# Optimization experiments

Hardware: AMD Instinct MI355X
Metric: run time of the kernel (lower is better)

## Reference

```python
import jax, jax.numpy as jnp
import numpy as np

D_MODEL = 4096
N_HEADS = 32
N_KV_HEADS = 8
HEAD_DIM = D_MODEL // N_HEADS  # 128
SEQ = 2048
BATCH = 1
ROPE_BASE = 10000.0


def build_rope_cache(max_seq_len, head_dim, base=10000.0):
    half = head_dim // 2
    pos = jnp.arange(max_seq_len, dtype=jnp.float32)
    inv_freqs = 1.0 / (base ** (jnp.arange(half, dtype=jnp.float32) / half))
    angles = pos[:, None] * inv_freqs[None, :]  # (S, half)
    return jnp.cos(angles), jnp.sin(angles)


def apply_rope(t, cos, sin):
    # t: (B, H, S, D); cos/sin: (S, D//2) broadcast over batch & heads.
    t_even = t[..., 0::2]
    t_odd = t[..., 1::2]
    c = cos[None, None, :, :]
    s = sin[None, None, :, :]
    rot_even = t_even * c - t_odd * s
    rot_odd = t_even * s + t_odd * c
    # interleave back into even/odd slots
    return jnp.stack([rot_even, rot_odd], axis=-1).reshape(t.shape)


def setup_inputs() -> dict:
    key = jax.random.key(0)
    kx, kq, kk, kv, ko = jax.random.split(key, 5)
    bound = 1.0 / np.sqrt(D_MODEL)
    x = jax.random.normal(kx, (BATCH, SEQ, D_MODEL), dtype=jnp.float32)
    # torch Linear weights: (out_features, in_features)
    wq = jax.random.uniform(kq, (N_HEADS * HEAD_DIM, D_MODEL), minval=-bound, maxval=bound, dtype=jnp.float32)
    wk = jax.random.uniform(kk, (N_KV_HEADS * HEAD_DIM, D_MODEL), minval=-bound, maxval=bound, dtype=jnp.float32)
    wv = jax.random.uniform(kv, (N_KV_HEADS * HEAD_DIM, D_MODEL), minval=-bound, maxval=bound, dtype=jnp.float32)
    wo = jax.random.uniform(ko, (D_MODEL, D_MODEL), minval=-bound, maxval=bound, dtype=jnp.float32)
    attn_mask = jnp.tril(jnp.ones((SEQ, SEQ), dtype=jnp.int32))[None, None, :, :]
    return {"x": x, "wq": wq, "wk": wk, "wv": wv, "wo": wo, "attn_mask": attn_mask}


def reference(x, wq, wk, wv, wo, attn_mask):
    B, S, _ = x.shape
    cos, sin = build_rope_cache(SEQ, HEAD_DIM, ROPE_BASE)
    cos, sin = cos[:S], sin[:S]
    q = (x @ wq.T).reshape(B, S, N_HEADS, HEAD_DIM).transpose(0, 2, 1, 3)      # (B,H,S,D)
    k = (x @ wk.T).reshape(B, S, N_KV_HEADS, HEAD_DIM).transpose(0, 2, 1, 3)   # (B,Hkv,S,D)
    v = (x @ wv.T).reshape(B, S, N_KV_HEADS, HEAD_DIM).transpose(0, 2, 1, 3)
    q = apply_rope(q, cos, sin)
    k = apply_rope(k, cos, sin)
    n_rep = N_HEADS // N_KV_HEADS
    if n_rep > 1:
        k = jnp.repeat(k, n_rep, axis=1)
        v = jnp.repeat(v, n_rep, axis=1)
    scores = jnp.einsum('bhqd,bhkd->bhqk', q, k) / jnp.sqrt(jnp.float32(HEAD_DIM))
    scores = jnp.where(attn_mask == 0, -jnp.inf, scores)
    attn = jax.nn.softmax(scores, axis=-1)
    out = jnp.einsum('bhqk,bhkd->bhqd', attn, v)
    out = out.transpose(0, 2, 1, 3).reshape(B, S, D_MODEL)
    return out @ wo.T
```

## Files before the change

### kernel.cpp

```cpp
#include <hip/hip_runtime.h>
#include <hip/hip_bf16.h>

typedef float f32x4 __attribute__((ext_vector_type(4)));
typedef __bf16 bf16x4 __attribute__((ext_vector_type(4)));
typedef __bf16 bf16x8 __attribute__((ext_vector_type(8)));

__device__ __forceinline__ void gld_lds16(const void* g, void* l) {
  __builtin_amdgcn_global_load_lds((const __attribute__((address_space(1))) void*)g,
                                   (__attribute__((address_space(3))) void*)l, 16, 0, 0);
}

__global__ void cvt_f32_bf16(const float* __restrict__ in, __bf16* __restrict__ out,
                             int n8) {
  int idx = blockIdx.x * blockDim.x + threadIdx.x;
  if (idx >= n8) return;
  f32x4 a = *(const f32x4*)(in + (size_t)idx * 8);
  f32x4 b = *(const f32x4*)(in + (size_t)idx * 8 + 4);
  bf16x8 o;
#pragma unroll
  for (int j = 0; j < 4; ++j) { o[j] = (__bf16)a[j]; o[4 + j] = (__bf16)b[j]; }
  *(bf16x8*)(out + (size_t)idx * 8) = o;
}

__global__ void build_trig(float* __restrict__ trig) {
  int idx = blockIdx.x * blockDim.x + threadIdx.x;
  if (idx >= 2048 * 64) return;
  int i = idx & 63, s = idx >> 6;
  float ang = (float)s * powf(10000.0f, -(float)i * (1.0f / 64.0f));
  float sn, cs;
  sincosf(ang, &sn, &cs);
  trig[idx * 2] = cs;
  trig[idx * 2 + 1] = sn;
}

__global__ void rope_bf16(__bf16* __restrict__ T, const float* __restrict__ trig,
                          int stride, int nh_mask, int nh_shift, float mul, int total) {
  int idx = blockIdx.x * blockDim.x + threadIdx.x;
  if (idx >= total) return;
  int i = idx & 63;
  int h = (idx >> 6) & nh_mask;
  int s = idx >> (6 + nh_shift);
  float cs = trig[(s * 64 + i) * 2];
  float sn = trig[(s * 64 + i) * 2 + 1];
  __bf16* p = T + (size_t)s * stride + h * 128 + 2 * i;
  float e = (float)p[0], o = (float)p[1];
  p[0] = (__bf16)((e * cs - o * sn) * mul);
  p[1] = (__bf16)((e * sn + o * cs) * mul);
}

__global__ __launch_bounds__(256) void transpose_v(const __bf16* __restrict__ KVb,
                                                   __bf16* __restrict__ Vt) {
  __shared__ __bf16 T[64][72];
  const int tid = threadIdx.x;
  const int s0 = blockIdx.x * 64, d0 = blockIdx.y * 64;
  const int r = tid >> 3, c8 = (tid & 7) * 8;
#pragma unroll
  for (int i = 0; i < 2; ++i) {
    int row = i * 32 + r;
    *(bf16x8*)&T[row][c8] = *(const bf16x8*)&KVb[(size_t)(s0 + row) * 2048 + 1024 + d0 + c8];
  }
  __syncthreads();
#pragma unroll
  for (int i = 0; i < 2; ++i) {
    int drow = i * 32 + r;
    bf16x8 o;
#pragma unroll
    for (int j = 0; j < 8; ++j) o[j] = T[c8 + j][drow];
    *(bf16x8*)&Vt[(size_t)(d0 + drow) * 2048 + s0 + c8] = o;
  }
}

template <int BM, int BN, typename OutT>
__global__ __launch_bounds__(256) void gemm_bf16(const __bf16* __restrict__ A,
                                                 const __bf16* __restrict__ B0,
                                                 const __bf16* __restrict__ B1,
                                                 int Nsplit, OutT* __restrict__ C,
                                                 int M, int N, int K) {
  constexpr int MI = BM / 32, NJ = BN / 32;
  constexpr int RA = BM / 32, RB = BN / 32;
  __shared__ __bf16 As[BM * 64] __attribute__((aligned(16)));
  __shared__ __bf16 Bs[BN * 64] __attribute__((aligned(16)));

  const int tid = threadIdx.x;
  const int lane = tid & 63;
  const int w = tid >> 6;
  const int nwg = gridDim.x * gridDim.y;
  const int orig = blockIdx.y * gridDim.x + blockIdx.x;
  const int wgid = (orig & 7) * (nwg >> 3) + (orig >> 3);
  const int m0 = (wgid % gridDim.x) * BM;
  const int n0 = (wgid / gridDim.x) * BN;
  const int li = lane & 15, lg = lane >> 4;

  const __bf16* bsrc[RB];
#pragma unroll
  for (int i = 0; i < RB; ++i) {
    int slot = i * 256 + w * 64 + lane;
    int row = slot >> 3;
    int sch = (slot & 7) ^ (row & 7);
    int n = n0 + row;
    bsrc[i] = (n < Nsplit ? B0 + (size_t)n * K : B1 + (size_t)(n - Nsplit) * K) +
              sch * 8;
  }
  const __bf16* asrc[RA];
#pragma unroll
  for (int i = 0; i < RA; ++i) {
    int slot = i * 256 + w * 64 + lane;
    int row = slot >> 3;
    int sch = (slot & 7) ^ (row & 7);
    asrc[i] = A + (size_t)(m0 + row) * K + sch * 8;
  }

  const int wr = (w >> 1) * (BM / 2);
  const int wc = (w & 1) * (BN / 2);

  f32x4 acc[MI][NJ] = {};

  for (int k0 = 0; k0 < K; k0 += 64) {
    __syncthreads();
#pragma unroll
    for (int i = 0; i < RA; ++i)
      gld_lds16(asrc[i] + k0, &As[(i * 256 + w * 64) * 8]);
#pragma unroll
    for (int i = 0; i < RB; ++i)
      gld_lds16(bsrc[i] + k0, &Bs[(i * 256 + w * 64) * 8]);
    __syncthreads();

#pragma unroll
    for (int u = 0; u < 2; ++u) {
      bf16x8 af[MI], bfr[NJ];
#pragma unroll
      for (int mi = 0; mi < MI; ++mi)
        af[mi] = *(const bf16x8*)&As[(wr + mi * 16 + li) * 64 +
                                     (((u * 4 + lg) ^ (li & 7)) * 8)];
#pragma unroll
      for (int nj = 0; nj < NJ; ++nj)
        bfr[nj] = *(const bf16x8*)&Bs[(wc + nj * 16 + li) * 64 +
                                      (((u * 4 + lg) ^ (li & 7)) * 8)];
#pragma unroll
      for (int mi = 0; mi < MI; ++mi)
#pragma unroll
        for (int nj = 0; nj < NJ; ++nj)
          acc[mi][nj] = __builtin_amdgcn_mfma_f32_16x16x32_bf16(af[mi], bfr[nj],
                                                                acc[mi][nj], 0, 0, 0);
    }
  }

  const int crow = lg * 4;
#pragma unroll
  for (int mi = 0; mi < MI; ++mi)
#pragma unroll
    for (int nj = 0; nj < NJ; ++nj)
#pragma unroll
      for (int r = 0; r < 4; ++r)
        C[(size_t)(m0 + wr + mi * 16 + crow + r) * N + (n0 + wc + nj * 16 + li)] =
            (OutT)acc[mi][nj][r];
}

__global__ __launch_bounds__(512) void attn_fwd_v6(const __bf16* __restrict__ Q,
                                                   const __bf16* __restrict__ KVb,
                                                   const __bf16* __restrict__ Vt,
                                                   __bf16* __restrict__ O) {
  const int tid = threadIdx.x;
  const int lane = tid & 63;
  const int w = tid >> 6;
  const int orig = blockIdx.x;
  const int chunk = orig & 7;
  const int wkk = orig >> 3;
  const int h = chunk * 4 + (wkk & 3);
  const int pair = wkk >> 2;
  const int kvh = h >> 2;

  __shared__ __bf16 Ks[2][64 * 128] __attribute__((aligned(16)));
  __shared__ __bf16 Vts[2][128 * 64] __attribute__((aligned(16)));
  __shared__ __bf16 Ps[8][16 * 72] __attribute__((aligned(16)));

  const int li = lane & 15, lg = lane >> 4;

  auto stage_k = [&](int k0, int buf) {
#pragma unroll
    for (int i = 0; i < 2; ++i) {
      int slot = i * 512 + tid;
      int row = slot >> 4;
      int sch = (slot & 15) ^ (row & 7);
      gld_lds16(&KVb[(size_t)(k0 + row) * 2048 + kvh * 128 + sch * 8],
                &Ks[buf][(i * 512 + w * 64) * 8]);
    }
  };
  auto stage_v = [&](int k0, int buf) {
#pragma unroll
    for (int i = 0; i < 2; ++i) {
      int slot = i * 512 + tid;
      int row = slot >> 3;
      int sch = (slot & 7) ^ (row & 7);
      gld_lds16(&Vt[(size_t)(kvh * 128 + row) * 2048 + k0 + sch * 8],
                &Vts[buf][(i * 512 + w * 64) * 8]);
    }
  };

#pragma unroll 1
  for (int pass = 0; pass < 2; ++pass) {
    const int m0 = ((pass == 0) ? (15 - pair) : pair) * 128;
    const int rbase = m0 + w * 16;

    bf16x8 qf[4];
    {
      const __bf16* qrow = Q + (size_t)(rbase + li) * 4096 + h * 128;
#pragma unroll
      for (int kc = 0; kc < 4; ++kc) qf[kc] = *(const bf16x8*)(qrow + kc * 32 + lg * 8);
    }

    f32x4 accO[8] = {};
    float plane = 0.f;

    const int wmax = rbase + 15;
    const int ntile = (m0 + 128) >> 6;

    __builtin_amdgcn_s_barrier();
    stage_v(0, 0);
    stage_k(0, 0);

#pragma unroll 1
    for (int t = 0; t < ntile; ++t) {
      const int k0 = t * 64;
      const int cur = t & 1;

      __builtin_amdgcn_s_barrier();
      const int nk = (t + 1 < ntile) ? k0 + 64 : 0;
      stage_v(nk, cur ^ 1);
      stage_k(nk, cur ^ 1);

      asm volatile("s_waitcnt vmcnt(4)" ::: "memory");
      __builtin_amdgcn_s_barrier();
      __builtin_amdgcn_sched_barrier(0);
      asm volatile("" ::: "memory");

      if (k0 <= wmax) {
        f32x4 s2[4] = {};
        __builtin_amdgcn_s_setprio(1);
#pragma unroll
        for (int nt = 0; nt < 4; ++nt)
#pragma unroll
          for (int kc = 0; kc < 4; ++kc) {
            bf16x8 kf = *(const bf16x8*)&Ks[cur][(li + 16 * nt) * 128 +
                                                (((4 * kc + lg) ^ (li & 7)) * 8)];
            s2[nt] = __builtin_amdgcn_mfma_f32_16x16x32_bf16(kf, qf[kc], s2[nt], 0, 0, 0);
          }
        __builtin_amdgcn_s_setprio(0);

        const int q = rbase + li;
        const bool needmask = (k0 + 63 > rbase);
#pragma unroll
        for (int nt = 0; nt < 4; ++nt) {
          bf16x4 pk;
#pragma unroll
          for (int r = 0; r < 4; ++r) {
            const int key = k0 + 16 * nt + lg * 4 + r;
            float v = s2[nt][r];
            if (needmask && key > q) v = -INFINITY;
            float p = exp2f(v);
            plane += p;
            pk[r] = (__bf16)p;
          }
          *(bf16x4*)&Ps[w][li * 72 + 16 * nt + lg * 4] = pk;
        }
        bf16x8 pa[2];
        pa[0] = *(const bf16x8*)&Ps[w][li * 72 + lg * 8];
        pa[1] = *(const bf16x8*)&Ps[w][li * 72 + 32 + lg * 8];

        __builtin_amdgcn_s_setprio(1);
#pragma unroll
        for (int dt = 0; dt < 8; ++dt)
#pragma unroll
          for (int kc = 0; kc < 2; ++kc) {
            bf16x8 vf = *(const bf16x8*)&Vts[cur][(li + 16 * dt) * 64 +
                                                 (((4 * kc + lg) ^ (li & 7)) * 8)];
            accO[dt] = __builtin_amdgcn_mfma_f32_16x16x32_bf16(pa[kc], vf, accO[dt], 0, 0, 0);
          }
        __builtin_amdgcn_s_setprio(0);
      }
    }

    {
      float sum = plane;
      sum += __shfl_xor(sum, 16);
      sum += __shfl_xor(sum, 32);
      float inv[4];
#pragma unroll
      for (int r = 0; r < 4; ++r) inv[r] = 1.0f / __shfl(sum, lg * 4 + r);
#pragma unroll
      for (int dt = 0; dt < 8; ++dt)
#pragma unroll
        for (int r = 0; r < 4; ++r)
          O[(size_t)(rbase + lg * 4 + r) * 4096 + h * 128 + dt * 16 + li] =
              (__bf16)(accO[dt][r] * inv[r]);
    }
  }
}

extern "C" void kernel_launch(void* const* d_in, const int* in_sizes, int n_in,
                              void* d_out, int out_size, void* d_ws, size_t ws_size,
                              hipStream_t stream) {
  const float* x  = (const float*)d_in[0];
  const float* wq = (const float*)d_in[1];
  const float* wk = (const float*)d_in[2];
  const float* wv = (const float*)d_in[3];
  const float* wo = (const float*)d_in[4];
  float* out = (float*)d_out;

  const int S = 2048, D = 4096;
  char* ws = (char*)d_ws;
  __bf16* xb  = (__bf16*)ws;
  __bf16* Qb  = (__bf16*)(ws + 16777216);
  __bf16* KVb = (__bf16*)(ws + 33554432);
  __bf16* Vt  = (__bf16*)(ws + 41943040);
  __bf16* wb  = (__bf16*)(ws + 46137344);
  float*  trig = (float*)(ws + 79691776);
  __bf16* AOb = xb;

  const float qscale = 0.08838834764831845f * 1.4426950408889634f;

  cvt_f32_bf16<<<(S * D / 8 + 255) / 256, 256, 0, stream>>>(x, xb, S * D / 8);
  cvt_f32_bf16<<<(D * D / 8 + 255) / 256, 256, 0, stream>>>(wq, wb, D * D / 8);
  gemm_bf16<128, 128, __bf16><<<dim3(16, 32), 256, 0, stream>>>(
      xb, wb, wb, 1 << 30, Qb, S, D, D);

  cvt_f32_bf16<<<(1024 * D / 8 + 255) / 256, 256, 0, stream>>>(wk, wb, 1024 * D / 8);
  cvt_f32_bf16<<<(1024 * D / 8 + 255) / 256, 256, 0, stream>>>(wv, wb + (size_t)1024 * D,
                                                               1024 * D / 8);
  gemm_bf16<64, 128, __bf16><<<dim3(32, 16), 256, 0, stream>>>(
      xb, wb, wb + (size_t)1024 * D, 1024, KVb, S, 2048, D);

  build_trig<<<(2048 * 64 + 255) / 256, 256, 0, stream>>>(trig);
  rope_bf16<<<(S * 32 * 64 + 255) / 256, 256, 0, stream>>>(Qb, trig, 4096, 31, 5,
                                                           qscale, S * 32 * 64);
  rope_bf16<<<(S * 8 * 64 + 255) / 256, 256, 0, stream>>>(KVb, trig, 2048, 7, 3,
                                                          1.0f, S * 8 * 64);
  transpose_v<<<dim3(32, 16), 256, 0, stream>>>(KVb, Vt);

  attn_fwd_v6<<<256, 512, 0, stream>>>(Qb, KVb, Vt, AOb);

  cvt_f32_bf16<<<(D * D / 8 + 255) / 256, 256, 0, stream>>>(wo, wb, D * D / 8);
  gemm_bf16<128, 128, float><<<dim3(16, 32), 256, 0, stream>>>(
      AOb, wb, wb, 1 << 30, out, S, D, D);
}
```

Baseline: 364.8 us.

## Add 256x128-tile 8-wave GEMM kernel for Q and output projections

Adds a new bf16 GEMM kernel that uses 256x128 output tiles per 512-thread workgroup. It double-buffers K-chunks of 64 into LDS via direct global-to-LDS loads with XOR swizzling and remaps workgroup ids across 8 groups. Each wave computes a 128x32 sub-tile, which raises MFMA work per LDS fragment load. The Q projection and the output projection now use it instead of the 128x128 kernel. This halves the workgroup count to 256, which lowers per-block A/B traffic but may leave some compute units underused and raises register pressure from 16 accumulators per lane.

```diff
diff --git a/kernel.cpp b/kernel.cpp
--- a/kernel.cpp
+++ b/kernel.cpp
@@ -156,6 +156,110 @@
             (OutT)acc[mi][nj][r];
 }
 
+template <typename OutT>
+__global__ __launch_bounds__(512) void gemm_bt8(const __bf16* __restrict__ A,
+                                                const __bf16* __restrict__ B,
+                                                OutT* __restrict__ C,
+                                                int M, int N, int K) {
+  __shared__ __bf16 As[2][256 * 64] __attribute__((aligned(16)));
+  __shared__ __bf16 Bs[2][128 * 64] __attribute__((aligned(16)));
+
+  const int tid = threadIdx.x;
+  const int lane = tid & 63;
+  const int w = tid >> 6;
+  const int nwg = gridDim.x * gridDim.y;
+  const int orig = blockIdx.y * gridDim.x + blockIdx.x;
+  const int wgid = (orig & 7) * (nwg >> 3) + (orig >> 3);
+  const int m0 = (wgid % gridDim.x) * 256;
+  const int n0 = (wgid / gridDim.x) * 128;
+  const int li = lane & 15, lg = lane >> 4;
+
+  const __bf16* asrc[4];
+#pragma unroll
+  for (int i = 0; i < 4; ++i) {
+    int slot = i * 512 + tid;
+    int row = slot >> 3;
+    int sch = (slot & 7) ^ (row & 7);
+    asrc[i] = A + (size_t)(m0 + row) * K + sch * 8;
+  }
+  const __bf16* bsrc[2];
+#pragma unroll
+  for (int i = 0; i < 2; ++i) {
+    int slot = i * 512 + tid;
+    int row = slot >> 3;
+    int sch = (slot & 7) ^ (row & 7);
+    bsrc[i] = B + (size_t)(n0 + row) * K + sch * 8;
+  }
+
+  auto stage = [&](int buf, int kt) {
+    const int k0 = kt * 64;
+#pragma unroll
+    for (int i = 0; i < 4; ++i)
+      gld_lds16(asrc[i] + k0, &As[buf][(i * 512 + w * 64) * 8]);
+#pragma unroll
+    for (int i = 0; i < 2; ++i)
+      gld_lds16(bsrc[i] + k0, &Bs[buf][(i * 512 + w * 64) * 8]);
+  };
+
+  const int wm = (w >> 2) * 128;
+  const int wn = (w & 3) * 32;
+
+  f32x4 acc[8][2] = {};
+  const int NT = K >> 6;
+
+  stage(0, 0);
+  stage(1, 1);
+  asm volatile("s_waitcnt vmcnt(6)" ::: "memory");
+  __builtin_amdgcn_s_barrier();
+  __builtin_amdgcn_sched_barrier(0);
+
+#pragma unroll 1
+  for (int t = 0; t < NT; ++t) {
+    const int cur = t & 1;
+
+#pragma unroll
+    for (int u = 0; u < 2; ++u) {
+      const int kc = ((u * 4 + lg) ^ (li & 7)) * 8;
+      bf16x8 af[8], bfr[2];
+#pragma unroll
+      for (int mi = 0; mi < 8; ++mi)
+        af[mi] = *(const bf16x8*)&As[cur][(wm + mi * 16 + li) * 64 + kc];
+#pragma unroll
+      for (int nj = 0; nj < 2; ++nj)
+        bfr[nj] = *(const bf16x8*)&Bs[cur][(wn + nj * 16 + li) * 64 + kc];
+      __builtin_amdgcn_s_setprio(1);
+#pragma unroll
+      for (int mi = 0; mi < 8; ++mi)
+#pragma unroll
+        for (int nj = 0; nj < 2; ++nj)
+          acc[mi][nj] = __builtin_amdgcn_mfma_f32_16x16x32_bf16(af[mi], bfr[nj],
+                                                                acc[mi][nj], 0, 0, 0);
+      __builtin_amdgcn_s_setprio(0);
+    }
+
+    __builtin_amdgcn_s_barrier();
+    __builtin_amdgcn_sched_barrier(0);
+
+    if (t + 2 < NT) {
+      stage(cur, t + 2);
+      asm volatile("s_waitcnt vmcnt(6)" ::: "memory");
+    } else {
+      asm volatile("s_waitcnt vmcnt(0)" ::: "memory");
+    }
+    __builtin_amdgcn_s_barrier();
+    __builtin_amdgcn_sched_barrier(0);
+  }
+
+#pragma unroll
+  for (int mi = 0; mi < 8; ++mi)
+#pragma unroll
+    for (int nj = 0; nj < 2; ++nj)
+#pragma unroll
+      for (int r = 0; r < 4; ++r)
+        C[(size_t)(m0 + wm + mi * 16 + lg * 4 + r) * N + (n0 + wn + nj * 16 + li)] =
+            (OutT)acc[mi][nj][r];
+}
+
 __global__ __launch_bounds__(512) void attn_fwd_v6(const __bf16* __restrict__ Q,
                                                    const __bf16* __restrict__ KVb,
                                                    const __bf16* __restrict__ Vt,
@@ -321,8 +425,7 @@
 
   cvt_f32_bf16<<<(S * D / 8 + 255) / 256, 256, 0, stream>>>(x, xb, S * D / 8);
   cvt_f32_bf16<<<(D * D / 8 + 255) / 256, 256, 0, stream>>>(wq, wb, D * D / 8);
-  gemm_bf16<128, 128, __bf16><<<dim3(16, 32), 256, 0, stream>>>(
-      xb, wb, wb, 1 << 30, Qb, S, D, D);
+  gemm_bt8<__bf16><<<dim3(8, 32), 512, 0, stream>>>(xb, wb, Qb, S, D, D);
 
   cvt_f32_bf16<<<(1024 * D / 8 + 255) / 256, 256, 0, stream>>>(wk, wb, 1024 * D / 8);
   cvt_f32_bf16<<<(1024 * D / 8 + 255) / 256, 256, 0, stream>>>(wv, wb + (size_t)1024 * D,
@@ -340,6 +443,5 @@
   attn_fwd_v6<<<256, 512, 0, stream>>>(Qb, KVb, Vt, AOb);
 
   cvt_f32_bf16<<<(D * D / 8 + 255) / 256, 256, 0, stream>>>(wo, wb, D * D / 8);
-  gemm_bf16<128, 128, float><<<dim3(16, 32), 256, 0, stream>>>(
-      AOb, wb, wb, 1 << 30, out, S, D, D);
-}
+  gemm_bt8<float><<<dim3(8, 32), 512, 0, stream>>>(AOb, wb, out, S, D, D);
+}
```

After: 386.0 us. 1.06x slower.

## Fuse Q RoPE into attention and switch to 64-row blocks with single V buffer

Applied to the files above, without the earlier changes.

The separate RoPE pass over Q is removed; the attention kernel now applies rotary embedding and the softmax scale to Q while loading it, using the precomputed trig table. The attention grid changes from 256 blocks of 512 threads, each doing two paired 128-row passes, to 1024 blocks of 256 threads covering 64 query rows each, ordered heaviest-first. V staging becomes single-buffered with an extra barrier and wait point inside the loop. This saves one full read-modify-write of Q and may improve load balance, but it adds barriers and drops the causal tile-skip check. There is also some redundant trig reading per block.

```diff
diff --git a/kernel.cpp b/kernel.cpp
--- a/kernel.cpp
+++ b/kernel.cpp
@@ -1,6 +1,7 @@
 #include <hip/hip_runtime.h>
 #include <hip/hip_bf16.h>
 
+typedef float f32x2 __attribute__((ext_vector_type(2)));
 typedef float f32x4 __attribute__((ext_vector_type(4)));
 typedef __bf16 bf16x4 __attribute__((ext_vector_type(4)));
 typedef __bf16 bf16x8 __attribute__((ext_vector_type(8)));
@@ -156,144 +157,149 @@
             (OutT)acc[mi][nj][r];
 }
 
-__global__ __launch_bounds__(512) void attn_fwd_v6(const __bf16* __restrict__ Q,
+__global__ __launch_bounds__(256) void attn_fwd_v7(const __bf16* __restrict__ Q,
                                                    const __bf16* __restrict__ KVb,
                                                    const __bf16* __restrict__ Vt,
+                                                   const float* __restrict__ trig,
                                                    __bf16* __restrict__ O) {
   const int tid = threadIdx.x;
   const int lane = tid & 63;
   const int w = tid >> 6;
-  const int orig = blockIdx.x;
-  const int chunk = orig & 7;
-  const int wkk = orig >> 3;
-  const int h = chunk * 4 + (wkk & 3);
-  const int pair = wkk >> 2;
+  const int bid = blockIdx.x;
+  const int xcd = bid & 7;
+  const int r9 = bid >> 3;
+  const int h = xcd * 4 + (r9 & 3);
+  const int mb = 31 - (r9 >> 2);
   const int kvh = h >> 2;
+  const int m0 = mb * 64;
+  const int rbase = m0 + w * 16;
 
   __shared__ __bf16 Ks[2][64 * 128] __attribute__((aligned(16)));
-  __shared__ __bf16 Vts[2][128 * 64] __attribute__((aligned(16)));
-  __shared__ __bf16 Ps[8][16 * 72] __attribute__((aligned(16)));
+  __shared__ __bf16 Vs[128 * 64] __attribute__((aligned(16)));
+  __shared__ __bf16 Ps[4][16 * 72] __attribute__((aligned(16)));
 
   const int li = lane & 15, lg = lane >> 4;
+  const float qscale = 0.08838834764831845f * 1.4426950408889634f;
 
   auto stage_k = [&](int k0, int buf) {
 #pragma unroll
-    for (int i = 0; i < 2; ++i) {
-      int slot = i * 512 + tid;
+    for (int i = 0; i < 4; ++i) {
+      int slot = i * 256 + tid;
       int row = slot >> 4;
       int sch = (slot & 15) ^ (row & 7);
       gld_lds16(&KVb[(size_t)(k0 + row) * 2048 + kvh * 128 + sch * 8],
-                &Ks[buf][(i * 512 + w * 64) * 8]);
+                &Ks[buf][(i * 256 + w * 64) * 8]);
     }
   };
-  auto stage_v = [&](int k0, int buf) {
-#pragma unroll
-    for (int i = 0; i < 2; ++i) {
-      int slot = i * 512 + tid;
+  auto stage_v = [&](int k0) {
+#pragma unroll
+    for (int i = 0; i < 4; ++i) {
+      int slot = i * 256 + tid;
       int row = slot >> 3;
       int sch = (slot & 7) ^ (row & 7);
       gld_lds16(&Vt[(size_t)(kvh * 128 + row) * 2048 + k0 + sch * 8],
-                &Vts[buf][(i * 512 + w * 64) * 8]);
+                &Vs[(i * 256 + w * 64) * 8]);
     }
   };
 
+  const int s = rbase + li;
+  bf16x8 qf[4];
+  {
+    const __bf16* qrow = Q + (size_t)s * 4096 + h * 128;
+#pragma unroll
+    for (int kc = 0; kc < 4; ++kc) {
+      bf16x8 raw = *(const bf16x8*)(qrow + kc * 32 + lg * 8);
+#pragma unroll
+      for (int jj = 0; jj < 4; ++jj) {
+        int i = kc * 16 + lg * 4 + jj;
+        f32x2 cs = *(const f32x2*)&trig[((size_t)s * 64 + i) * 2];
+        float e = (float)raw[2 * jj], o = (float)raw[2 * jj + 1];
+        qf[kc][2 * jj]     = (__bf16)((e * cs[0] - o * cs[1]) * qscale);
+        qf[kc][2 * jj + 1] = (__bf16)((e * cs[1] + o * cs[0]) * qscale);
+      }
+    }
+  }
+
+  f32x4 accO[8] = {};
+  float plane = 0.f;
+  const int ntile = mb + 1;
+
+  stage_k(0, 0);
+
 #pragma unroll 1
-  for (int pass = 0; pass < 2; ++pass) {
-    const int m0 = ((pass == 0) ? (15 - pair) : pair) * 128;
-    const int rbase = m0 + w * 16;
-
-    bf16x8 qf[4];
-    {
-      const __bf16* qrow = Q + (size_t)(rbase + li) * 4096 + h * 128;
-#pragma unroll
-      for (int kc = 0; kc < 4; ++kc) qf[kc] = *(const bf16x8*)(qrow + kc * 32 + lg * 8);
-    }
-
-    f32x4 accO[8] = {};
-    float plane = 0.f;
-
-    const int wmax = rbase + 15;
-    const int ntile = (m0 + 128) >> 6;
-
+  for (int t = 0; t < ntile; ++t) {
+    const int k0 = t * 64;
+    const int cur = t & 1;
+    stage_v(k0);
+    stage_k(t + 1 < ntile ? k0 + 64 : 0, cur ^ 1);
+
+    asm volatile("s_waitcnt vmcnt(8)" ::: "memory");
     __builtin_amdgcn_s_barrier();
-    stage_v(0, 0);
-    stage_k(0, 0);
-
-#pragma unroll 1
-    for (int t = 0; t < ntile; ++t) {
-      const int k0 = t * 64;
-      const int cur = t & 1;
-
-      __builtin_amdgcn_s_barrier();
-      const int nk = (t + 1 < ntile) ? k0 + 64 : 0;
-      stage_v(nk, cur ^ 1);
-      stage_k(nk, cur ^ 1);
-
-      asm volatile("s_waitcnt vmcnt(4)" ::: "memory");
-      __builtin_amdgcn_s_barrier();
-      __builtin_amdgcn_sched_barrier(0);
-      asm volatile("" ::: "memory");
-
-      if (k0 <= wmax) {
-        f32x4 s2[4] = {};
-        __builtin_amdgcn_s_setprio(1);
-#pragma unroll
-        for (int nt = 0; nt < 4; ++nt)
-#pragma unroll
-          for (int kc = 0; kc < 4; ++kc) {
-            bf16x8 kf = *(const bf16x8*)&Ks[cur][(li + 16 * nt) * 128 +
-                                                (((4 * kc + lg) ^ (li & 7)) * 8)];
-            s2[nt] = __builtin_amdgcn_mfma_f32_16x16x32_bf16(kf, qf[kc], s2[nt], 0, 0, 0);
-          }
-        __builtin_amdgcn_s_setprio(0);
-
-        const int q = rbase + li;
-        const bool needmask = (k0 + 63 > rbase);
-#pragma unroll
-        for (int nt = 0; nt < 4; ++nt) {
-          bf16x4 pk;
-#pragma unroll
-          for (int r = 0; r < 4; ++r) {
-            const int key = k0 + 16 * nt + lg * 4 + r;
-            float v = s2[nt][r];
-            if (needmask && key > q) v = -INFINITY;
-            float p = exp2f(v);
-            plane += p;
-            pk[r] = (__bf16)p;
-          }
-          *(bf16x4*)&Ps[w][li * 72 + 16 * nt + lg * 4] = pk;
-        }
-        bf16x8 pa[2];
-        pa[0] = *(const bf16x8*)&Ps[w][li * 72 + lg * 8];
-        pa[1] = *(const bf16x8*)&Ps[w][li * 72 + 32 + lg * 8];
-
-        __builtin_amdgcn_s_setprio(1);
-#pragma unroll
-        for (int dt = 0; dt < 8; ++dt)
-#pragma unroll
-          for (int kc = 0; kc < 2; ++kc) {
-            bf16x8 vf = *(const bf16x8*)&Vts[cur][(li + 16 * dt) * 64 +
-                                                 (((4 * kc + lg) ^ (li & 7)) * 8)];
-            accO[dt] = __builtin_amdgcn_mfma_f32_16x16x32_bf16(pa[kc], vf, accO[dt], 0, 0, 0);
-          }
-        __builtin_amdgcn_s_setprio(0);
+    __builtin_amdgcn_sched_barrier(0);
+
+    f32x4 s2[4] = {};
+    __builtin_amdgcn_s_setprio(1);
+#pragma unroll
+    for (int nt = 0; nt < 4; ++nt)
+#pragma unroll
+      for (int kc = 0; kc < 4; ++kc) {
+        bf16x8 kf = *(const bf16x8*)&Ks[cur][(li + 16 * nt) * 128 +
+                                            (((4 * kc + lg) ^ (li & 7)) * 8)];
+        s2[nt] = __builtin_amdgcn_mfma_f32_16x16x32_bf16(kf, qf[kc], s2[nt], 0, 0, 0);
       }
-    }
-
-    {
-      float sum = plane;
-      sum += __shfl_xor(sum, 16);
-      sum += __shfl_xor(sum, 32);
-      float inv[4];
-#pragma unroll
-      for (int r = 0; r < 4; ++r) inv[r] = 1.0f / __shfl(sum, lg * 4 + r);
-#pragma unroll
-      for (int dt = 0; dt < 8; ++dt)
-#pragma unroll
-        for (int r = 0; r < 4; ++r)
-          O[(size_t)(rbase + lg * 4 + r) * 4096 + h * 128 + dt * 16 + li] =
-              (__bf16)(accO[dt][r] * inv[r]);
-    }
+    __builtin_amdgcn_s_setprio(0);
+
+    const bool needmask = (k0 + 63 > rbase);
+#pragma unroll
+    for (int nt = 0; nt < 4; ++nt) {
+      bf16x4 pk;
+#pragma unroll
+      for (int rr = 0; rr < 4; ++rr) {
+        const int key = k0 + 16 * nt + lg * 4 + rr;
+        float v = s2[nt][rr];
+        if (needmask && key > s) v = -INFINITY;
+        float p = exp2f(v);
+        plane += p;
+        pk[rr] = (__bf16)p;
+      }
+      *(bf16x4*)&Ps[w][li * 72 + 16 * nt + lg * 4] = pk;
+    }
+    bf16x8 pa[2];
+    pa[0] = *(const bf16x8*)&Ps[w][li * 72 + lg * 8];
+    pa[1] = *(const bf16x8*)&Ps[w][li * 72 + 32 + lg * 8];
+
+    asm volatile("s_waitcnt vmcnt(4)" ::: "memory");
+    __builtin_amdgcn_s_barrier();
+    __builtin_amdgcn_sched_barrier(0);
+
+    __builtin_amdgcn_s_setprio(1);
+#pragma unroll
+    for (int dt = 0; dt < 8; ++dt)
+#pragma unroll
+      for (int kc = 0; kc < 2; ++kc) {
+        bf16x8 vf = *(const bf16x8*)&Vs[(li + 16 * dt) * 64 +
+                                        (((4 * kc + lg) ^ (li & 7)) * 8)];
+        accO[dt] = __builtin_amdgcn_mfma_f32_16x16x32_bf16(pa[kc], vf, accO[dt], 0, 0, 0);
+      }
+    __builtin_amdgcn_s_setprio(0);
+
+    __builtin_amdgcn_s_barrier();
+    __builtin_amdgcn_sched_barrier(0);
+  }
+
+  {
+    float sum = plane;
+    sum += __shfl_xor(sum, 16);
+    sum += __shfl_xor(sum, 32);
+    float inv[4];
+#pragma unroll
+    for (int rr = 0; rr < 4; ++rr) inv[rr] = 1.0f / __shfl(sum, lg * 4 + rr);
+#pragma unroll
+    for (int dt = 0; dt < 8; ++dt)
+#pragma unroll
+      for (int rr = 0; rr < 4; ++rr)
+        O[(size_t)(rbase + lg * 4 + rr) * 4096 + h * 128 + dt * 16 + li] =
+            (__bf16)(accO[dt][rr] * inv[rr]);
   }
 }
 
@@ -317,8 +323,6 @@
   float*  trig = (float*)(ws + 79691776);
   __bf16* AOb = xb;
 
-  const float qscale = 0.08838834764831845f * 1.4426950408889634f;
-
   cvt_f32_bf16<<<(S * D / 8 + 255) / 256, 256, 0, stream>>>(x, xb, S * D / 8);
   cvt_f32_bf16<<<(D * D / 8 + 255) / 256, 256, 0, stream>>>(wq, wb, D * D / 8);
   gemm_bf16<128, 128, __bf16><<<dim3(16, 32), 256, 0, stream>>>(
@@ -331,13 +335,11 @@
       xb, wb, wb + (size_t)1024 * D, 1024, KVb, S, 2048, D);
 
   build_trig<<<(2048 * 64 + 255) / 256, 256, 0, stream>>>(trig);
-  rope_bf16<<<(S * 32 * 64 + 255) / 256, 256, 0, stream>>>(Qb, trig, 4096, 31, 5,
-                                                           qscale, S * 32 * 64);
   rope_bf16<<<(S * 8 * 64 + 255) / 256, 256, 0, stream>>>(KVb, trig, 2048, 7, 3,
                                                           1.0f, S * 8 * 64);
   transpose_v<<<dim3(32, 16), 256, 0, stream>>>(KVb, Vt);
 
-  attn_fwd_v6<<<256, 512, 0, stream>>>(Qb, KVb, Vt, AOb);
+  attn_fwd_v7<<<1024, 256, 0, stream>>>(Qb, KVb, Vt, trig, AOb);
 
   cvt_f32_bf16<<<(D * D / 8 + 255) / 256, 256, 0, stream>>>(wo, wb, D * D / 8);
   gemm_bf16<128, 128, float><<<dim3(16, 32), 256, 0, stream>>>(
```

New measurement: 344.7 us. 1.06x faster.
